# Kernel optimization log

Measured on AMD Instinct MI355X. Metric: run time of the kernel, lower is better.

The kernel has to match this reference:

```python
import jax, jax.numpy as jnp
import numpy as np

CELL = 128
STEPS = 20
N_KEYS = 4   # ['first_conn','second_conn','first_op','second_op']
N_OUT = 6


def setup_inputs() -> dict:
    key = jax.random.key(0)
    ks = jax.random.split(key, 10)
    s = 0.05
    return {
        "net": jax.random.randint(ks[0], (STEPS,), 0, N_OUT),          # sampled actions, each in [0,6)
        "reward": jax.random.uniform(ks[1], (1,), dtype=jnp.float32),   # unused in forward (kept for signature parity)
        "emb_start": jax.random.normal(ks[2], (1, CELL), jnp.float32) * s,          # Embedding(1,128)
        "emb_keys": jax.random.normal(ks[3], (N_KEYS, N_OUT, CELL), jnp.float32) * s,
        "fc_W": jax.random.normal(ks[4], (N_KEYS, N_OUT, CELL), jnp.float32) * s,
        "fc_b": jax.random.normal(ks[5], (N_KEYS, N_OUT), jnp.float32) * s,
        "W_ih": jax.random.normal(ks[6], (4 * CELL, CELL), jnp.float32) * s,  # LSTMCell input weights (i,f,g,o)
        "W_hh": jax.random.normal(ks[7], (4 * CELL, CELL), jnp.float32) * s,  # LSTMCell hidden weights
        "b_ih": jax.random.normal(ks[8], (4 * CELL,), jnp.float32) * s,
        "b_hh": jax.random.normal(ks[9], (4 * CELL,), jnp.float32) * s,
    }


def _lstm_cell(x, h, c, W_ih, W_hh, b_ih, b_hh):
    # PyTorch LSTMCell: gates ordered (i, f, g, o)
    gates = x @ W_ih.T + b_ih + h @ W_hh.T + b_hh   # [1, 4*CELL]
    i, f, g, o = jnp.split(gates, 4, axis=-1)
    c_new = jax.nn.sigmoid(f) * c + jax.nn.sigmoid(i) * jnp.tanh(g)
    h_new = jax.nn.sigmoid(o) * jnp.tanh(c_new)
    return h_new, c_new


def reference(net, reward, emb_start, emb_keys, fc_W, fc_b, W_ih, W_hh, b_ih, b_hh):
    key_idx = jnp.arange(STEPS) % N_KEYS            # which head/embedding at each step
    fc_W_t = fc_W[key_idx]                          # [STEPS, 6, CELL]
    fc_b_t = fc_b[key_idx]                          # [STEPS, 6]
    emb_t = emb_keys[key_idx, net]                  # [STEPS, CELL] next-step input embedding

    def step(carry, xs):
        h, c, x = carry
        Wt, bt, ev = xs
        h, c = _lstm_cell(x, h, c, W_ih, W_hh, b_ih, b_hh)
        probs = jax.nn.softmax(h @ Wt.T + bt, axis=1)   # [1, 6]
        return (h, c, ev[None, :]), probs

    h0 = jnp.zeros((1, CELL), dtype=emb_start.dtype)
    c0 = jnp.zeros((1, CELL), dtype=emb_start.dtype)
    x0 = emb_start                                   # embedding lookup of action 0 in a 1-row table
    _, outputs = jax.lax.scan(step, (h0, c0, x0), (fc_W_t, fc_b_t, emb_t))
    return outputs                                   # [STEPS, 1, 6], stacked version of the torch list
```

## Files before the change

### kernel.cpp

```cpp
#include <hip/hip_runtime.h>
#include <hip/hip_fp16.h>

#define CELL 128
#define STEPS 20

typedef _Float16 half8_t __attribute__((ext_vector_type(8)));
typedef float    floatx4 __attribute__((ext_vector_type(4)));

__device__ __forceinline__ unsigned packf2(float x, float y) {
    typedef _Float16 h2 __attribute__((ext_vector_type(2)));
    h2 h = { (_Float16)x, (_Float16)y };
    return __builtin_bit_cast(unsigned, h);
}

__device__ __forceinline__ float fast_sigmoid(float x) { return 1.0f / (1.0f + __expf(-x)); }
__device__ __forceinline__ float fast_tanh(float x) {
    return 2.0f / (1.0f + __expf(-2.0f * x)) - 1.0f;
}

extern "C" __global__ void __launch_bounds__(1024, 1)
nas_policy_kernel(const int* __restrict__ net,
                  const float* __restrict__ emb_start,
                  const float* __restrict__ emb_keys,
                  const float* __restrict__ fc_W,
                  const float* __restrict__ fc_b,
                  const float* __restrict__ W_ih,
                  const float* __restrict__ W_hh,
                  const float* __restrict__ b_ih,
                  const float* __restrict__ b_hh,
                  float* __restrict__ out)
{
    const int t0   = threadIdx.x;
    const int wv   = t0 >> 6;
    const int lane = t0 & 63;
    const int quad = lane >> 4;
    const int lcol = lane & 15;

    __shared__ __align__(16) unsigned xh2[2 * 64];
    __shared__ __align__(16) unsigned s_embk2[24 * 64];
    __shared__ float h_f32[CELL];
    __shared__ float gates[4 * CELL];
    __shared__ float s_fcW[24 * CELL];
    __shared__ float s_fcb[24];
    __shared__ float logits[8];
    __shared__ int   s_net[STEPS];

    const int r1 = (wv << 5) + lcol;
    const int r2 = r1 + 16;
    half8_t bf1[8], bf2[8];
#pragma unroll
    for (int kc = 0; kc < 8; ++kc) {
        const int k0 = (kc << 5) + (quad << 3);
        const float* s1 = (k0 < 128) ? (W_ih + r1 * CELL + k0) : (W_hh + r1 * CELL + (k0 - 128));
        const float* s2 = (k0 < 128) ? (W_ih + r2 * CELL + k0) : (W_hh + r2 * CELL + (k0 - 128));
        float4 a = ((const float4*)s1)[0], b = ((const float4*)s1)[1];
        bf1[kc] = half8_t{ (_Float16)a.x, (_Float16)a.y, (_Float16)a.z, (_Float16)a.w,
                           (_Float16)b.x, (_Float16)b.y, (_Float16)b.z, (_Float16)b.w };
        a = ((const float4*)s2)[0]; b = ((const float4*)s2)[1];
        bf2[kc] = half8_t{ (_Float16)a.x, (_Float16)a.y, (_Float16)a.z, (_Float16)a.w,
                           (_Float16)b.x, (_Float16)b.y, (_Float16)b.z, (_Float16)b.w };
    }
    const float bias1 = b_ih[r1] + b_hh[r1];
    const float bias2 = b_ih[r2] + b_hh[r2];

    {
        const float2* ek2 = (const float2*)emb_keys;
        for (int i = t0; i < 24 * 64; i += 1024) {
            float2 v = ek2[i];
            s_embk2[i] = packf2(v.x, v.y);
        }
        for (int i = t0; i < 24 * CELL; i += 1024) s_fcW[i] = fc_W[i];
        if (t0 < 24)    s_fcb[t0] = fc_b[t0];
        if (t0 < STEPS) s_net[t0] = net[t0];
        if (t0 < 64) {
            float2 v = ((const float2*)emb_start)[t0];
            xh2[t0]      = packf2(v.x, v.y);
            xh2[64 + t0] = 0u;
        }
    }
    float c = 0.0f;

    for (int t = 0; t < STEPS; ++t) {
        __syncthreads();

        if (t > 0 && t0 < 6) {
            float l0 = logits[0], l1 = logits[1], l2 = logits[2];
            float l3 = logits[3], l4 = logits[4], l5 = logits[5];
            float m = fmaxf(fmaxf(fmaxf(l0, l1), fmaxf(l2, l3)), fmaxf(l4, l5));
            float e0 = __expf(l0 - m), e1 = __expf(l1 - m), e2 = __expf(l2 - m);
            float e3 = __expf(l3 - m), e4 = __expf(l4 - m), e5 = __expf(l5 - m);
            float s = ((e0 + e1) + (e2 + e3)) + (e4 + e5);
            float mine = (t0 == 0) ? e0 : (t0 == 1) ? e1 : (t0 == 2) ? e2
                       : (t0 == 3) ? e3 : (t0 == 4) ? e4 : e5;
            out[(t - 1) * 6 + t0] = mine / s;
        }

        floatx4 acc1 = { 0.f, 0.f, 0.f, 0.f };
        floatx4 acc2 = { 0.f, 0.f, 0.f, 0.f };
        const uint4* xp = (const uint4*)xh2;
#pragma unroll
        for (int kc = 0; kc < 8; ++kc) {
            uint4 u = xp[(kc << 2) + quad];
            half8_t af = __builtin_bit_cast(half8_t, u);
            acc1 = __builtin_amdgcn_mfma_f32_16x16x32_f16(af, bf1[kc], acc1, 0, 0, 0);
            acc2 = __builtin_amdgcn_mfma_f32_16x16x32_f16(af, bf2[kc], acc2, 0, 0, 0);
        }
        if (lane < 16) {
            gates[(wv << 5) + lane]      = acc1[0] + bias1;
            gates[(wv << 5) + 16 + lane] = acc2[0] + bias2;
        }

        __syncthreads();

        if (t0 < CELL) {
            float ig = fast_sigmoid(gates[t0]);
            float fg = fast_sigmoid(gates[CELL + t0]);
            float gg = fast_tanh   (gates[2 * CELL + t0]);
            float og = fast_sigmoid(gates[3 * CELL + t0]);
            c = fg * c + ig * gg;
            h_f32[t0] = og * fast_tanh(c);
        }

        __syncthreads();

        if (wv < 6) {
            const float* Wr = s_fcW + (((t & 3) * 6) + wv) * CELL;
            float p2 = h_f32[lane]      * Wr[lane]
                     + h_f32[64 + lane] * Wr[64 + lane];
#pragma unroll
            for (int off = 32; off >= 1; off >>= 1) p2 += __shfl_down(p2, off);
            if (lane == 0) logits[wv] = p2 + s_fcb[(t & 3) * 6 + wv];
        } else if (wv == 6) {
            xh2[64 + lane] = packf2(h_f32[2 * lane], h_f32[2 * lane + 1]);
        } else if (wv == 7) {
            xh2[lane] = s_embk2[(((t & 3) * 6) + s_net[t]) * 64 + lane];
        }
    }

    __syncthreads();
    if (t0 < 6) {
        float l0 = logits[0], l1 = logits[1], l2 = logits[2];
        float l3 = logits[3], l4 = logits[4], l5 = logits[5];
        float m = fmaxf(fmaxf(fmaxf(l0, l1), fmaxf(l2, l3)), fmaxf(l4, l5));
        float e0 = __expf(l0 - m), e1 = __expf(l1 - m), e2 = __expf(l2 - m);
        float e3 = __expf(l3 - m), e4 = __expf(l4 - m), e5 = __expf(l5 - m);
        float s = ((e0 + e1) + (e2 + e3)) + (e4 + e5);
        float mine = (t0 == 0) ? e0 : (t0 == 1) ? e1 : (t0 == 2) ? e2
                   : (t0 == 3) ? e3 : (t0 == 4) ? e4 : e5;
        out[(STEPS - 1) * 6 + t0] = mine / s;
    }
}

extern "C" void kernel_launch(void* const* d_in, const int* in_sizes, int n_in,
                              void* d_out, int out_size, void* d_ws, size_t ws_size,
                              hipStream_t stream) {
    (void)in_sizes; (void)n_in; (void)out_size; (void)d_ws; (void)ws_size;
    const int*   net       = (const int*)d_in[0];
    const float* emb_start = (const float*)d_in[2];
    const float* emb_keys  = (const float*)d_in[3];
    const float* fc_W      = (const float*)d_in[4];
    const float* fc_b      = (const float*)d_in[5];
    const float* W_ih      = (const float*)d_in[6];
    const float* W_hh      = (const float*)d_in[7];
    const float* b_ih      = (const float*)d_in[8];
    const float* b_hh      = (const float*)d_in[9];
    float*       out       = (float*)d_out;

    hipLaunchKernelGGL(nas_policy_kernel, dim3(1), dim3(1024), 0, stream,
                       net, emb_start, emb_keys, fc_W, fc_b,
                       W_ih, W_hh, b_ih, b_hh, out);
}
```

Baseline: 108.8 us.

## Halve block size and software-pipeline FC head to drop a barrier per step

Result: no change. 110.4 us (+1.4%).

```diff
diff --git a/kernel.cpp b/kernel.cpp
--- a/kernel.cpp
+++ b/kernel.cpp
@@ -12,13 +12,21 @@
     h2 h = { (_Float16)x, (_Float16)y };
     return __builtin_bit_cast(unsigned, h);
 }
+__device__ __forceinline__ float h2lo(unsigned u) {
+    typedef _Float16 h2 __attribute__((ext_vector_type(2)));
+    h2 h = __builtin_bit_cast(h2, u); return (float)h[0];
+}
+__device__ __forceinline__ float h2hi(unsigned u) {
+    typedef _Float16 h2 __attribute__((ext_vector_type(2)));
+    h2 h = __builtin_bit_cast(h2, u); return (float)h[1];
+}
 
 __device__ __forceinline__ float fast_sigmoid(float x) { return 1.0f / (1.0f + __expf(-x)); }
 __device__ __forceinline__ float fast_tanh(float x) {
     return 2.0f / (1.0f + __expf(-2.0f * x)) - 1.0f;
 }
 
-extern "C" __global__ void __launch_bounds__(1024, 1)
+extern "C" __global__ void __launch_bounds__(512, 1)
 nas_policy_kernel(const int* __restrict__ net,
                   const float* __restrict__ emb_start,
                   const float* __restrict__ emb_keys,
@@ -38,38 +46,39 @@
 
     __shared__ __align__(16) unsigned xh2[2 * 64];
     __shared__ __align__(16) unsigned s_embk2[24 * 64];
-    __shared__ float h_f32[CELL];
     __shared__ float gates[4 * CELL];
     __shared__ float s_fcW[24 * CELL];
     __shared__ float s_fcb[24];
-    __shared__ float logits[8];
+    __shared__ float logits[2 * 8];
     __shared__ int   s_net[STEPS];
 
-    const int r1 = (wv << 5) + lcol;
-    const int r2 = r1 + 16;
-    half8_t bf1[8], bf2[8];
+    const int rbase = wv << 6;
+    const int r0 = rbase + lcol, r1 = r0 + 16, r2 = r0 + 32, r3 = r0 + 48;
+    half8_t bf0[8], bf1[8], bf2[8], bf3[8];
 #pragma unroll
     for (int kc = 0; kc < 8; ++kc) {
         const int k0 = (kc << 5) + (quad << 3);
-        const float* s1 = (k0 < 128) ? (W_ih + r1 * CELL + k0) : (W_hh + r1 * CELL + (k0 - 128));
-        const float* s2 = (k0 < 128) ? (W_ih + r2 * CELL + k0) : (W_hh + r2 * CELL + (k0 - 128));
-        float4 a = ((const float4*)s1)[0], b = ((const float4*)s1)[1];
-        bf1[kc] = half8_t{ (_Float16)a.x, (_Float16)a.y, (_Float16)a.z, (_Float16)a.w,
-                           (_Float16)b.x, (_Float16)b.y, (_Float16)b.z, (_Float16)b.w };
-        a = ((const float4*)s2)[0]; b = ((const float4*)s2)[1];
-        bf2[kc] = half8_t{ (_Float16)a.x, (_Float16)a.y, (_Float16)a.z, (_Float16)a.w,
-                           (_Float16)b.x, (_Float16)b.y, (_Float16)b.z, (_Float16)b.w };
-    }
+        const float* base = (k0 < 128) ? W_ih + k0 : W_hh + (k0 - 128);
+#define LD8(dst, row) { \
+        const float4* p4 = (const float4*)(base + (row) * CELL); \
+        float4 a = p4[0], b = p4[1]; \
+        dst = half8_t{ (_Float16)a.x, (_Float16)a.y, (_Float16)a.z, (_Float16)a.w, \
+                       (_Float16)b.x, (_Float16)b.y, (_Float16)b.z, (_Float16)b.w }; }
+        LD8(bf0[kc], r0) LD8(bf1[kc], r1) LD8(bf2[kc], r2) LD8(bf3[kc], r3)
+#undef LD8
+    }
+    const float bias0 = b_ih[r0] + b_hh[r0];
     const float bias1 = b_ih[r1] + b_hh[r1];
     const float bias2 = b_ih[r2] + b_hh[r2];
+    const float bias3 = b_ih[r3] + b_hh[r3];
 
     {
         const float2* ek2 = (const float2*)emb_keys;
-        for (int i = t0; i < 24 * 64; i += 1024) {
+        for (int i = t0; i < 24 * 64; i += 512) {
             float2 v = ek2[i];
             s_embk2[i] = packf2(v.x, v.y);
         }
-        for (int i = t0; i < 24 * CELL; i += 1024) s_fcW[i] = fc_W[i];
+        for (int i = t0; i < 24 * CELL; i += 512) s_fcW[i] = fc_W[i];
         if (t0 < 24)    s_fcb[t0] = fc_b[t0];
         if (t0 < STEPS) s_net[t0] = net[t0];
         if (t0 < 64) {
@@ -83,31 +92,45 @@
     for (int t = 0; t < STEPS; ++t) {
         __syncthreads();
 
-        if (t > 0 && t0 < 6) {
-            float l0 = logits[0], l1 = logits[1], l2 = logits[2];
-            float l3 = logits[3], l4 = logits[4], l5 = logits[5];
+        floatx4 acc0 = {0,0,0,0}, acc1 = {0,0,0,0}, acc2 = {0,0,0,0}, acc3 = {0,0,0,0};
+        const uint4* xp = (const uint4*)xh2;
+#pragma unroll
+        for (int kc = 0; kc < 8; ++kc) {
+            uint4 u = xp[(kc << 2) + quad];
+            half8_t af = __builtin_bit_cast(half8_t, u);
+            acc0 = __builtin_amdgcn_mfma_f32_16x16x32_f16(af, bf0[kc], acc0, 0, 0, 0);
+            acc1 = __builtin_amdgcn_mfma_f32_16x16x32_f16(af, bf1[kc], acc1, 0, 0, 0);
+            acc2 = __builtin_amdgcn_mfma_f32_16x16x32_f16(af, bf2[kc], acc2, 0, 0, 0);
+            acc3 = __builtin_amdgcn_mfma_f32_16x16x32_f16(af, bf3[kc], acc3, 0, 0, 0);
+        }
+        if (lane < 16) {
+            gates[rbase + lane]      = acc0[0] + bias0;
+            gates[rbase + 16 + lane] = acc1[0] + bias1;
+            gates[rbase + 32 + lane] = acc2[0] + bias2;
+            gates[rbase + 48 + lane] = acc3[0] + bias3;
+        }
+
+        if (t >= 1 && wv < 6) {
+            const int ti = t - 1;
+            unsigned hu = xh2[64 + lane];
+            const float* Wr = s_fcW + (((ti & 3) * 6) + wv) * CELL;
+            float p2 = h2lo(hu) * Wr[2 * lane] + h2hi(hu) * Wr[2 * lane + 1];
+#pragma unroll
+            for (int off = 32; off >= 1; off >>= 1) p2 += __shfl_down(p2, off);
+            if (lane == 0)
+                logits[((ti & 1) << 3) + wv] = p2 + s_fcb[(ti & 3) * 6 + wv];
+        }
+
+        if (t >= 2 && t0 < 6) {
+            const float* L = logits + ((t & 1) << 3);
+            float l0 = L[0], l1 = L[1], l2 = L[2], l3 = L[3], l4 = L[4], l5 = L[5];
             float m = fmaxf(fmaxf(fmaxf(l0, l1), fmaxf(l2, l3)), fmaxf(l4, l5));
             float e0 = __expf(l0 - m), e1 = __expf(l1 - m), e2 = __expf(l2 - m);
             float e3 = __expf(l3 - m), e4 = __expf(l4 - m), e5 = __expf(l5 - m);
             float s = ((e0 + e1) + (e2 + e3)) + (e4 + e5);
             float mine = (t0 == 0) ? e0 : (t0 == 1) ? e1 : (t0 == 2) ? e2
                        : (t0 == 3) ? e3 : (t0 == 4) ? e4 : e5;
-            out[(t - 1) * 6 + t0] = mine / s;
-        }
-
-        floatx4 acc1 = { 0.f, 0.f, 0.f, 0.f };
-        floatx4 acc2 = { 0.f, 0.f, 0.f, 0.f };
-        const uint4* xp = (const uint4*)xh2;
-#pragma unroll
-        for (int kc = 0; kc < 8; ++kc) {
-            uint4 u = xp[(kc << 2) + quad];
-            half8_t af = __builtin_bit_cast(half8_t, u);
-            acc1 = __builtin_amdgcn_mfma_f32_16x16x32_f16(af, bf1[kc], acc1, 0, 0, 0);
-            acc2 = __builtin_amdgcn_mfma_f32_16x16x32_f16(af, bf2[kc], acc2, 0, 0, 0);
-        }
-        if (lane < 16) {
-            gates[(wv << 5) + lane]      = acc1[0] + bias1;
-            gates[(wv << 5) + 16 + lane] = acc2[0] + bias2;
+            out[(t - 2) * 6 + t0] = mine / s;
         }
 
         __syncthreads();
@@ -118,36 +141,46 @@
             float gg = fast_tanh   (gates[2 * CELL + t0]);
             float og = fast_sigmoid(gates[3 * CELL + t0]);
             c = fg * c + ig * gg;
-            h_f32[t0] = og * fast_tanh(c);
-        }
-
-        __syncthreads();
-
-        if (wv < 6) {
-            const float* Wr = s_fcW + (((t & 3) * 6) + wv) * CELL;
-            float p2 = h_f32[lane]      * Wr[lane]
-                     + h_f32[64 + lane] * Wr[64 + lane];
-#pragma unroll
-            for (int off = 32; off >= 1; off >>= 1) p2 += __shfl_down(p2, off);
-            if (lane == 0) logits[wv] = p2 + s_fcb[(t & 3) * 6 + wv];
-        } else if (wv == 6) {
-            xh2[64 + lane] = packf2(h_f32[2 * lane], h_f32[2 * lane + 1]);
-        } else if (wv == 7) {
-            xh2[lane] = s_embk2[(((t & 3) * 6) + s_net[t]) * 64 + lane];
+            float h = og * fast_tanh(c);
+            float hp = __shfl_xor(h, 1);
+            if ((t0 & 1) == 0)
+                xh2[64 + (t0 >> 1)] = packf2(h, hp);
+        } else if (wv == 2 && t < STEPS - 1) {
+            xh2[lane] = s_embk2[((((t + 1) & 3) * 6) + s_net[t + 1]) * 64 + lane];
         }
     }
 
     __syncthreads();
+    if (wv < 6) {
+        unsigned hu = xh2[64 + lane];
+        const float* Wr = s_fcW + (((19 & 3) * 6) + wv) * CELL;
+        float p2 = h2lo(hu) * Wr[2 * lane] + h2hi(hu) * Wr[2 * lane + 1];
+#pragma unroll
+        for (int off = 32; off >= 1; off >>= 1) p2 += __shfl_down(p2, off);
+        if (lane == 0) logits[((19 & 1) << 3) + wv] = p2 + s_fcb[(19 & 3) * 6 + wv];
+    }
     if (t0 < 6) {
-        float l0 = logits[0], l1 = logits[1], l2 = logits[2];
-        float l3 = logits[3], l4 = logits[4], l5 = logits[5];
+        const float* L = logits + ((18 & 1) << 3);
+        float l0 = L[0], l1 = L[1], l2 = L[2], l3 = L[3], l4 = L[4], l5 = L[5];
         float m = fmaxf(fmaxf(fmaxf(l0, l1), fmaxf(l2, l3)), fmaxf(l4, l5));
         float e0 = __expf(l0 - m), e1 = __expf(l1 - m), e2 = __expf(l2 - m);
         float e3 = __expf(l3 - m), e4 = __expf(l4 - m), e5 = __expf(l5 - m);
         float s = ((e0 + e1) + (e2 + e3)) + (e4 + e5);
         float mine = (t0 == 0) ? e0 : (t0 == 1) ? e1 : (t0 == 2) ? e2
                    : (t0 == 3) ? e3 : (t0 == 4) ? e4 : e5;
-        out[(STEPS - 1) * 6 + t0] = mine / s;
+        out[18 * 6 + t0] = mine / s;
+    }
+    __syncthreads();
+    if (t0 < 6) {
+        const float* L = logits + ((19 & 1) << 3);
+        float l0 = L[0], l1 = L[1], l2 = L[2], l3 = L[3], l4 = L[4], l5 = L[5];
+        float m = fmaxf(fmaxf(fmaxf(l0, l1), fmaxf(l2, l3)), fmaxf(l4, l5));
+        float e0 = __expf(l0 - m), e1 = __expf(l1 - m), e2 = __expf(l2 - m);
+        float e3 = __expf(l3 - m), e4 = __expf(l4 - m), e5 = __expf(l5 - m);
+        float s = ((e0 + e1) + (e2 + e3)) + (e4 + e5);
+        float mine = (t0 == 0) ? e0 : (t0 == 1) ? e1 : (t0 == 2) ? e2
+                   : (t0 == 3) ? e3 : (t0 == 4) ? e4 : e5;
+        out[19 * 6 + t0] = mine / s;
     }
 }
 
@@ -166,7 +199,7 @@
     const float* b_hh      = (const float*)d_in[9];
     float*       out       = (float*)d_out;
 
-    hipLaunchKernelGGL(nas_policy_kernel, dim3(1), dim3(1024), 0, stream,
+    hipLaunchKernelGGL(nas_policy_kernel, dim3(1), dim3(512), 0, stream,
                        net, emb_start, emb_keys, fc_W, fc_b,
                        W_ih, W_hh, b_ih, b_hh, out);
 }
```
